# Performance work log

Measured on AMD Instinct MI355X. Metric: run time of the kernel, lower is better.

The kernel has to match this reference:

```python
import jax, jax.numpy as jnp
import numpy as np

N, C, I, E = 2048, 128, 9, 10   # nodes, channels, num_ell (0e+1o+2e -> 1+3+5), elements
K3, K2, K1 = 23, 8, 3           # CG path counts per correlation order (synthetic)
D0, D1 = 1, 3                   # output irrep dims: 0e, 1o


def setup_inputs() -> dict:
    rng = np.random.default_rng(0)
    f = lambda *s: jnp.asarray(rng.standard_normal(s).astype(np.float32))
    elem = rng.integers(0, E, size=N)
    node_attrs = jnp.asarray(np.eye(E, dtype=np.float32)[elem])  # one-hot element types
    return {
        "node_feats": f(N, C, I),
        "sc": 0.1 * f(N, C * (D0 + D1)),
        "node_attrs": node_attrs,
        # generalized CG U-matrices per output irrep and correlation order (buffers)
        "U3_0": 0.1 * f(D0, I, I, I, K3), "U2_0": 0.1 * f(D0, I, I, K2), "U1_0": 0.1 * f(D0, I, K1),
        "W3_0": 0.1 * f(E, K3, C), "W2_0": 0.1 * f(E, K2, C), "W1_0": 0.1 * f(E, K1, C),
        "U3_1": 0.1 * f(D1, I, I, I, K3), "U2_1": 0.1 * f(D1, I, I, K2), "U1_1": 0.1 * f(D1, I, K1),
        "W3_1": 0.1 * f(E, K3, C), "W2_1": 0.1 * f(E, K2, C), "W1_1": 0.1 * f(E, K1, C),
        # equivariant Linear weights (one [mul_in, mul_out] block per output irrep)
        "Wlin0": f(C, C), "Wlin1": f(C, C),
    }


def _sym_contract(x, y, U3, U2, U1, W3, W2, W1):
    """MACE Contraction for one output irrep (correlation=3).
    x: [N,C,I] node features; y: [N,E] one-hot element attrs.
    Mirrors equations '...ik,ekc,bci,be->bc...', '...k,ekc,be->bc...', 'bc...i,bci->bc...'.
    """
    out = jnp.einsum("dpqik,ekc,nci,ne->ncdpq", U3, W3, x, y)   # corr-3 main term [N,C,d,I,I]
    out = out + jnp.einsum("dpqk,ekc,ne->ncdpq", U2, W2, y)     # add corr-2 weighting
    out = jnp.einsum("ncdpq,ncq->ncdp", out, x)                 # contract one feature index
    out = out + jnp.einsum("dpk,ekc,ne->ncdp", U1, W1, y)       # add corr-1 weighting
    out = jnp.einsum("ncdp,ncp->ncd", out, x)                   # final contraction -> [N,C,d]
    return out


def reference(node_feats, sc, node_attrs, U3_0, U2_0, U1_0, W3_0, W2_0, W1_0,
              U3_1, U2_1, U1_1, W3_1, W2_1, W1_1, Wlin0, Wlin1):
    n = node_feats.shape[0]
    f0 = _sym_contract(node_feats, node_attrs, U3_0, U2_0, U1_0, W3_0, W2_0, W1_0)  # [N,C,1]
    f1 = _sym_contract(node_feats, node_attrs, U3_1, U2_1, U1_1, W3_1, W2_1, W1_1)  # [N,C,3]
    inv = 1.0 / jnp.sqrt(jnp.asarray(C, node_feats.dtype))  # e3nn Linear fan-in normalization
    y0 = jnp.einsum("nud,uw->nwd", f0, Wlin0) * inv
    y1 = jnp.einsum("nud,uw->nwd", f1, Wlin1) * inv
    out = jnp.concatenate([y0.reshape(n, -1), y1.reshape(n, -1)], axis=-1)  # [N, C*(1+3)]
    return out + sc
```

## Files before the change

kernel.cpp:

```cpp
#include <hip/hip_runtime.h>

namespace {
constexpr int N_ = 2048, C_ = 128, I_ = 9, E_ = 10;
constexpr int NSLAB = 40;
constexpr int M_ = 8;
constexpr int NCHUNK = 64;
constexpr int NT3 = 165;
constexpr int NT2 = 45;

constexpr int O_ORDER = 0;
constexpr int O_BOFF  = N_;
constexpr int O_A     = N_ + 16;
constexpr int S_A     = NSLAB * 12 * C_ * 4;
constexpr int O_B     = O_A + S_A;
constexpr int S_B     = NSLAB * 42 * C_ * 4;
constexpr int O_C     = O_B + S_B;
constexpr int S_C     = NSLAB * 3 * C_ * 4;
constexpr int O_F     = O_C + S_C;
constexpr int NB_VPRE = 1160;
constexpr int NB_PREP = NB_VPRE + 8;
}

__device__ __forceinline__ float f4lane(float4 v, int l) {
  return l == 0 ? v.x : l == 1 ? v.y : l == 2 ? v.z : v.w;
}

__global__ __launch_bounds__(256) void prep_kernel(
    const float* __restrict__ attrs,
    const float* __restrict__ U3_0, const float* __restrict__ U2_0, const float* __restrict__ U1_0,
    const float* __restrict__ W3_0, const float* __restrict__ W2_0, const float* __restrict__ W1_0,
    const float* __restrict__ U3_1, const float* __restrict__ U2_1, const float* __restrict__ U1_1,
    const float* __restrict__ W3_1, const float* __restrict__ W2_1, const float* __restrict__ W1_1,
    float* __restrict__ ws_f, int* __restrict__ ws_i) {
  int bid = blockIdx.x;
  int t = threadIdx.x;

  if (bid < NB_VPRE) {
    int xcd = bid & 7, j = bid >> 3;
    int sg = j / 29, xp = j % 29;
    int slab = xcd + 8 * sg;
    int e = slab >> 2, dsel = slab & 3;
    int d = dsel ? dsel - 1 : 0;
    const float* U3 = dsel ? U3_1 : U3_0;
    const float* U2 = dsel ? U2_1 : U2_0;
    const float* U1 = dsel ? U1_1 : U1_0;
    const float* W3 = dsel ? W3_1 : W3_0;
    const float* W2 = dsel ? W2_1 : W2_0;
    const float* W1 = dsel ? W1_1 : W1_0;
    int half = t >> 7, c = t & 127;
    __shared__ float sf[8][23];

    if (xp < 21) {
      if (t < 184) {
        int s8 = t / 23, k = t % 23;
        int tt = 8 * xp + s8;
        float v = 0.f;
        if (tt < NT3) {
          int rem = tt, p = 0;
          for (;;) { int tp = (9 - p) * (10 - p) / 2; if (rem < tp) break; rem -= tp; ++p; }
          int q = p;
          for (;;) { int ln = 9 - q; if (rem < ln) break; rem -= ln; ++q; }
          int i = q + rem;
          auto u3 = [&](int a, int b, int g) {
            return U3[(((d * 9 + a) * 9 + b) * 9 + g) * 23 + k];
          };
          if (p == q && q == i)  v = u3(p, p, p);
          else if (p == q)       v = u3(p, p, i) + u3(p, i, p) + u3(i, p, p);
          else if (q == i)       v = u3(p, q, q) + u3(q, p, q) + u3(q, q, p);
          else                   v = u3(p, q, i) + u3(p, i, q) + u3(q, p, i)
                                   + u3(q, i, p) + u3(i, p, q) + u3(i, q, p);
        }
        sf[s8][k] = v;
      }
      __syncthreads();
      int sidx = 2 * xp + half;
      float acc[4] = {0.f, 0.f, 0.f, 0.f};
      for (int k = 0; k < 23; ++k) {
        float w = W3[(e * 23 + k) * C_ + c];
        #pragma unroll
        for (int l = 0; l < 4; ++l) acc[l] = fmaf(sf[half * 4 + l][k], w, acc[l]);
      }
      ((float4*)(ws_f + O_B))[((size_t)slab * 42 + sidx) * C_ + c] =
          make_float4(acc[0], acc[1], acc[2], acc[3]);
    } else if (xp < 27) {
      if (t < 64) {
        int s8 = t / 8, k = t % 8;
        int jj = 8 * (xp - 21) + s8;
        float v = 0.f;
        if (jj < NT2) {
          int rem = jj, p = 0;
          while (rem >= 9 - p) { rem -= 9 - p; ++p; }
          int q = p + rem;
          auto u2 = [&](int a, int b) { return U2[((d * 9 + a) * 9 + b) * 8 + k]; };
          v = (p == q) ? u2(p, p) : u2(p, q) + u2(q, p);
        }
        sf[s8][k] = v;
      }
      __syncthreads();
      int a = 2 * (xp - 21) + half;
      float acc[4] = {0.f, 0.f, 0.f, 0.f};
      for (int k = 0; k < 8; ++k) {
        float w = W2[(e * 8 + k) * C_ + c];
        #pragma unroll
        for (int l = 0; l < 4; ++l) acc[l] = fmaf(sf[half * 4 + l][k], w, acc[l]);
      }
      ((float4*)(ws_f + O_A))[((size_t)slab * 12 + a) * C_ + c] =
          make_float4(acc[0], acc[1], acc[2], acc[3]);
    } else {
      int ci, p0;
      if (xp == 27) { ci = half; p0 = 4 * half; }
      else { if (half) return; ci = 2; p0 = 8; }
      float acc[4] = {0.f, 0.f, 0.f, 0.f};
      for (int k = 0; k < 3; ++k) {
        float w = W1[(e * 3 + k) * C_ + c];
        #pragma unroll
        for (int l = 0; l < 4; ++l)
          if (p0 + l < 9) acc[l] = fmaf(U1[(d * 9 + p0 + l) * 3 + k], w, acc[l]);
      }
      ((float4*)(ws_f + O_C))[((size_t)slab * 3 + ci) * C_ + c] =
          make_float4(acc[0], acc[1], acc[2], acc[3]);
    }
  } else if (bid == NB_VPRE) {
    __shared__ int cnt[E_], base_s[E_ + 1], cur[E_];
    __shared__ short elem_s[N_];
    if (t < E_) cnt[t] = 0;
    __syncthreads();
    for (int n = t; n < N_; n += 256) {
      const float* a = attrs + n * E_;
      int best = 0; float bv = a[0];
      for (int e = 1; e < E_; ++e) { float v = a[e]; if (v > bv) { bv = v; best = e; } }
      elem_s[n] = (short)best;
      atomicAdd(&cnt[best], 1);
    }
    __syncthreads();
    if (t == 0) {
      int s = 0;
      for (int e = 0; e < E_; ++e) { base_s[e] = s; cur[e] = s; s += cnt[e]; }
      base_s[E_] = s;
    }
    __syncthreads();
    for (int n = t; n < N_; n += 256) {
      int p = atomicAdd(&cur[elem_s[n]], 1);
      ws_i[O_ORDER + p] = n;
    }
    if (t <= E_) ws_i[O_BOFF + t] = base_s[t];
  }
}

__device__ __forceinline__ void accum_all(const float4* __restrict__ A4,
                                          const float4* __restrict__ B4,
                                          const float4* __restrict__ C4,
                                          const float (&xm)[M_][I_], float (&f)[M_]) {
  #pragma unroll
  for (int p = 0; p < 9; ++p) {
    #pragma unroll
    for (int q = p; q < 9; ++q) {
      const int j  = 45 - (9 - p) * (10 - p) / 2 + (q - p);
      const int tb = 165 - (9 - p) * (10 - p) * (11 - p) / 6
                   + (9 - p) * (10 - p) / 2 - (9 - q) * (10 - q) / 2 - q;
      float s2 = f4lane(A4[(j >> 2) * C_], j & 3);
      float tv[M_];
      #pragma unroll
      for (int m = 0; m < M_; ++m) tv[m] = s2;
      #pragma unroll
      for (int i = q; i < 9; ++i) {
        const int tt = tb + i;
        float v = f4lane(B4[(tt >> 2) * C_], tt & 3);
        #pragma unroll
        for (int m = 0; m < M_; ++m) tv[m] = fmaf(xm[m][i], v, tv[m]);
      }
      #pragma unroll
      for (int m = 0; m < M_; ++m)
        f[m] = fmaf(xm[m][p] * xm[m][q], tv[m], f[m]);
    }
  }
  #pragma unroll
  for (int p = 0; p < 9; ++p) {
    float v = f4lane(C4[(p >> 2) * C_], p & 3);
    #pragma unroll
    for (int m = 0; m < M_; ++m) f[m] = fmaf(xm[m][p], v, f[m]);
  }
}

__global__ __launch_bounds__(128) void contract11_kernel(
    const float* __restrict__ x, const float* __restrict__ ws_f,
    const int* __restrict__ ws_i, float* __restrict__ fbuf) {
  int bid = blockIdx.x;
  int xcd = bid & 7;
  int sg  = (bid >> 3) % 5;
  int chunk = bid / 40;
  int slab = xcd + 8 * sg;
  int e = slab >> 2, dsel = slab & 3;
  int b0 = ws_i[O_BOFF + e];
  int cnt_e = ws_i[O_BOFF + e + 1] - b0;
  int base = chunk * M_;
  if (base >= cnt_e) return;
  int cnt = cnt_e - base; if (cnt > M_) cnt = M_;
  int c = threadIdx.x;

  const float4* A4 = (const float4*)(ws_f + O_A) + (size_t)slab * 12 * C_ + c;
  const float4* B4 = (const float4*)(ws_f + O_B) + (size_t)slab * 42 * C_ + c;
  const float4* C4 = (const float4*)(ws_f + O_C) + (size_t)slab * 3 * C_ + c;

  int nn[M_];
  #pragma unroll
  for (int m = 0; m < M_; ++m) {
    int idx = base + m; if (idx >= cnt_e) idx = cnt_e - 1;
    nn[m] = ws_i[O_ORDER + b0 + idx];
  }
  float xm[M_][I_];
  #pragma unroll
  for (int m = 0; m < M_; ++m) {
    const float* xp = x + ((size_t)nn[m] * C_ + c) * I_;
    #pragma unroll
    for (int i = 0; i < I_; ++i) xm[m][i] = xp[i];
  }
  float f[M_];
  #pragma unroll
  for (int m = 0; m < M_; ++m) f[m] = 0.f;

  accum_all(A4, B4, C4, xm, f);

  #pragma unroll
  for (int m = 0; m < M_; ++m)
    if (m < cnt) fbuf[((size_t)nn[m] * 4 + dsel) * C_ + c] = f[m];
}

__global__ __launch_bounds__(128) void linear3_kernel(
    const float* __restrict__ fbuf, const float* __restrict__ Wlin0,
    const float* __restrict__ Wlin1, const float* __restrict__ sc,
    float* __restrict__ out) {
  constexpr int NB = 8;
  int dt = blockIdx.y;
  int nb = blockIdx.x * NB;
  int w = threadIdx.x;
  __shared__ float fs[NB][C_];
  constexpr float inv = 0.08838834764831843f;
  #pragma unroll
  for (int r = 0; r < NB; ++r) fs[r][w] = fbuf[((nb + r) * 4 + dt) * C_ + w];
  __syncthreads();
  const float* Wl = (dt == 0) ? Wlin0 : Wlin1;
  float acc[NB];
  #pragma unroll
  for (int r = 0; r < NB; ++r) acc[r] = 0.f;
  for (int u = 0; u < C_; ++u) {
    float wv = Wl[u * C_ + w];
    #pragma unroll
    for (int r = 0; r < NB; ++r) acc[r] = fmaf(fs[r][u], wv, acc[r]);
  }
  if (dt == 0) {
    #pragma unroll
    for (int r = 0; r < NB; ++r) { int o = (nb + r) * 512 + w; out[o] = acc[r] * inv + sc[o]; }
  } else {
    int col = 128 + w * 3 + (dt - 1);
    #pragma unroll
    for (int r = 0; r < NB; ++r) { int o = (nb + r) * 512 + col; out[o] = acc[r] * inv + sc[o]; }
  }
}

extern "C" void kernel_launch(void* const* d_in, const int* in_sizes, int n_in,
                              void* d_out, int out_size, void* d_ws, size_t ws_size,
                              hipStream_t stream) {
  const float* node_feats = (const float*)d_in[0];
  const float* sc         = (const float*)d_in[1];
  const float* node_attrs = (const float*)d_in[2];
  const float* U3_0 = (const float*)d_in[3];
  const float* U2_0 = (const float*)d_in[4];
  const float* U1_0 = (const float*)d_in[5];
  const float* W3_0 = (const float*)d_in[6];
  const float* W2_0 = (const float*)d_in[7];
  const float* W1_0 = (const float*)d_in[8];
  const float* U3_1 = (const float*)d_in[9];
  const float* U2_1 = (const float*)d_in[10];
  const float* U1_1 = (const float*)d_in[11];
  const float* W3_1 = (const float*)d_in[12];
  const float* W2_1 = (const float*)d_in[13];
  const float* W1_1 = (const float*)d_in[14];
  const float* Wlin0 = (const float*)d_in[15];
  const float* Wlin1 = (const float*)d_in[16];

  float* ws_f = (float*)d_ws;
  int*   ws_i = (int*)d_ws;

  prep_kernel<<<NB_PREP, 256, 0, stream>>>(
      node_attrs,
      U3_0, U2_0, U1_0, W3_0, W2_0, W1_0,
      U3_1, U2_1, U1_1, W3_1, W2_1, W1_1, ws_f, ws_i);

  contract11_kernel<<<NSLAB * NCHUNK, 128, 0, stream>>>(
      node_feats, ws_f, ws_i, ws_f + O_F);

  linear3_kernel<<<dim3(N_ / 8, 4), 128, 0, stream>>>(
      ws_f + O_F, Wlin0, Wlin1, sc, (float*)d_out);
}
```

Before: 44.63 us.

## Fuse the equivariant linear layer into the contraction kernel epilogue

The separate linear3 kernel is removed. Each contraction block now stages its 8 per-node results in shared memory, applies the 128x128 Wlin matrix for its output irrep component, adds sc and writes the final output directly. This drops one kernel launch and the intermediate fbuf write and read through global memory. In exchange, the contraction kernel gains shared-memory use, a barrier and a 128-iteration matvec loop, which may raise register pressure and lower occupancy.

```diff
diff --git a/kernel.cpp b/kernel.cpp
--- a/kernel.cpp
+++ b/kernel.cpp
@@ -16,7 +16,6 @@
 constexpr int S_B     = NSLAB * 42 * C_ * 4;
 constexpr int O_C     = O_B + S_B;
 constexpr int S_C     = NSLAB * 3 * C_ * 4;
-constexpr int O_F     = O_C + S_C;
 constexpr int NB_VPRE = 1160;
 constexpr int NB_PREP = NB_VPRE + 8;
 }
@@ -182,9 +181,11 @@
   }
 }
 
-__global__ __launch_bounds__(128) void contract11_kernel(
+__global__ __launch_bounds__(128) void contract12_kernel(
     const float* __restrict__ x, const float* __restrict__ ws_f,
-    const int* __restrict__ ws_i, float* __restrict__ fbuf) {
+    const int* __restrict__ ws_i,
+    const float* __restrict__ Wlin0, const float* __restrict__ Wlin1,
+    const float* __restrict__ sc, float* __restrict__ out) {
   int bid = blockIdx.x;
   int xcd = bid & 7;
   int sg  = (bid >> 3) % 5;
@@ -221,40 +222,28 @@
 
   accum_all(A4, B4, C4, xm, f);
 
-  #pragma unroll
-  for (int m = 0; m < M_; ++m)
-    if (m < cnt) fbuf[((size_t)nn[m] * 4 + dsel) * C_ + c] = f[m];
-}
-
-__global__ __launch_bounds__(128) void linear3_kernel(
-    const float* __restrict__ fbuf, const float* __restrict__ Wlin0,
-    const float* __restrict__ Wlin1, const float* __restrict__ sc,
-    float* __restrict__ out) {
-  constexpr int NB = 8;
-  int dt = blockIdx.y;
-  int nb = blockIdx.x * NB;
-  int w = threadIdx.x;
-  __shared__ float fs[NB][C_];
+  __shared__ float fs[M_][C_ + 1];
+  #pragma unroll
+  for (int m = 0; m < M_; ++m) fs[m][c] = f[m];
+  __syncthreads();
+
+  const float* Wl = (dsel == 0) ? Wlin0 : Wlin1;
+  float acc[M_];
+  #pragma unroll
+  for (int m = 0; m < M_; ++m) acc[m] = 0.f;
+  for (int u = 0; u < C_; ++u) {
+    float wv = Wl[u * C_ + c];
+    #pragma unroll
+    for (int m = 0; m < M_; ++m) acc[m] = fmaf(fs[m][u], wv, acc[m]);
+  }
   constexpr float inv = 0.08838834764831843f;
-  #pragma unroll
-  for (int r = 0; r < NB; ++r) fs[r][w] = fbuf[((nb + r) * 4 + dt) * C_ + w];
-  __syncthreads();
-  const float* Wl = (dt == 0) ? Wlin0 : Wlin1;
-  float acc[NB];
-  #pragma unroll
-  for (int r = 0; r < NB; ++r) acc[r] = 0.f;
-  for (int u = 0; u < C_; ++u) {
-    float wv = Wl[u * C_ + w];
-    #pragma unroll
-    for (int r = 0; r < NB; ++r) acc[r] = fmaf(fs[r][u], wv, acc[r]);
-  }
-  if (dt == 0) {
-    #pragma unroll
-    for (int r = 0; r < NB; ++r) { int o = (nb + r) * 512 + w; out[o] = acc[r] * inv + sc[o]; }
-  } else {
-    int col = 128 + w * 3 + (dt - 1);
-    #pragma unroll
-    for (int r = 0; r < NB; ++r) { int o = (nb + r) * 512 + col; out[o] = acc[r] * inv + sc[o]; }
+  int col = (dsel == 0) ? c : C_ + c * 3 + (dsel - 1);
+  #pragma unroll
+  for (int m = 0; m < M_; ++m) {
+    if (m < cnt) {
+      int o = nn[m] * 512 + col;
+      out[o] = acc[m] * inv + sc[o];
+    }
   }
 }
 
@@ -287,9 +276,6 @@
       U3_0, U2_0, U1_0, W3_0, W2_0, W1_0,
       U3_1, U2_1, U1_1, W3_1, W2_1, W1_1, ws_f, ws_i);
 
-  contract11_kernel<<<NSLAB * NCHUNK, 128, 0, stream>>>(
-      node_feats, ws_f, ws_i, ws_f + O_F);
-
-  linear3_kernel<<<dim3(N_ / 8, 4), 128, 0, stream>>>(
-      ws_f + O_F, Wlin0, Wlin1, sc, (float*)d_out);
-}
+  contract12_kernel<<<NSLAB * NCHUNK, 128, 0, stream>>>(
+      node_feats, ws_f, ws_i, Wlin0, Wlin1, sc, (float*)d_out);
+}
```

New measurement: 42.92 us. 3.8% less time.
